# Kernel optimization log

Measured on AMD Instinct MI355X. Metric: run time of the kernel, lower is better.

Reference implementation:

```python
import jax, jax.numpy as jnp
import numpy as np

NEG_BIG = -9e15
ALPHA = 0.2  # leaky relu slope


def gat_layer(h, mask, W, a, concat):
    # h: [N, Fin], W: [Fin, Fout], a: [2*Fout], mask: [N, N] bool
    Wh = h @ W                                   # [N, Fout]
    d = W.shape[1]
    f1 = Wh @ a[:d]                              # [N]
    f2 = Wh @ a[d:]                              # [N]
    e = jax.nn.leaky_relu(f1[:, None] + f2[None, :], ALPHA)   # [N, N]
    e = jnp.where(mask, e, NEG_BIG)
    attn = jax.nn.softmax(e, axis=1)             # masked softmax over neighbors
    out = attn @ Wh                              # [N, Fout]
    return jax.nn.elu(out) if concat else out


def setup_inputs() -> dict:
    key = jax.random.key(0)
    ks = jax.random.split(key, 16)
    N, NFEAT, NHID, NCLASS, DEG_MAX, NHEADS = 4096, 512, 64, 16, 128, 8
    s = lambda fan_in: 1.0 / np.sqrt(fan_in)
    return {
        "x": jax.random.normal(ks[0], (N, NFEAT), jnp.float32),
        "adj": jax.random.randint(ks[1], (N, N), 0, 2, jnp.int32),
        "W_att": jax.random.normal(ks[2], (NHEADS, NFEAT, NHID), jnp.float32) * s(NFEAT),
        "a_att": jax.random.normal(ks[3], (NHEADS, 2 * NHID), jnp.float32) * s(2 * NHID),
        "W_out1": jax.random.normal(ks[4], (NHEADS * NHID, NCLASS), jnp.float32) * s(NHEADS * NHID),
        "a_out1": jax.random.normal(ks[5], (2 * NCLASS,), jnp.float32) * s(2 * NCLASS),
        "W_out2": jax.random.normal(ks[6], (NHEADS * NHID, NHID), jnp.float32) * s(NHEADS * NHID),
        "a_out2": jax.random.normal(ks[7], (2 * NHID,), jnp.float32) * s(2 * NHID),
        "W_down": jax.random.normal(ks[8], (NFEAT, NHID), jnp.float32) * s(NFEAT),
        "b_down": jnp.zeros((NHID,), jnp.float32),
        "w_deg": jax.random.normal(ks[9], (NHID, 1), jnp.float32) * s(NHID),
        "b_deg": jnp.zeros((1,), jnp.float32),
        "W_deg3": jax.random.normal(ks[10], (NHID, DEG_MAX), jnp.float32) * s(NHID),
        "b_deg3": jnp.zeros((DEG_MAX,), jnp.float32),
    }


def reference(x, adj, W_att, a_att, W_out1, a_out1, W_out2, a_out2,
              W_down, b_down, w_deg, b_deg, W_deg3, b_deg3):
    mask = adj > 0                                              # [N, N] bool
    original_x = x @ W_down + b_down                            # [N, nhid]
    # multi-head attention (dropout is identity in eval mode)
    heads = jax.vmap(lambda W, a: gat_layer(x, mask, W, a, True))(W_att, a_att)  # [H, N, nhid]
    h = jnp.transpose(heads, (1, 0, 2)).reshape(x.shape[0], -1)  # [N, H*nhid] == torch.cat(dim=1)
    classify_x = jax.nn.elu(gat_layer(h, mask, W_out1, a_out1, False))  # [N, nclass]
    z = gat_layer(h, mask, W_out2, a_out2, False) + original_x          # [N, nhid]
    result1 = jax.nn.log_softmax(classify_x, axis=1)            # [N, nclass]
    result2 = (z @ w_deg + b_deg)[:, 0]                         # [N]
    result3 = z @ W_deg3 + b_deg3                               # [N, degree_max]
    return (result1, result2, result3)
```

## Files before the change

kernel.cpp:

```cpp
#include <hip/hip_runtime.h>
#include <hip/hip_bf16.h>

#define L2E 1.44269504088896f

typedef __attribute__((ext_vector_type(8))) short short8v;
typedef __attribute__((ext_vector_type(8))) _Float16 half8v;
typedef __attribute__((ext_vector_type(4))) float float4v;

__device__ __forceinline__ void gld16(void* lds, const void* gp) {
    __builtin_amdgcn_global_load_lds(
        (const __attribute__((address_space(1))) unsigned int*)gp,
        (__attribute__((address_space(3))) unsigned int*)lds, 16, 0, 0);
}
__device__ __forceinline__ unsigned pkbf(float a, float b) {
    unsigned r;
    asm("v_cvt_pk_bf16_f32 %0, %1, %2" : "=v"(r) : "v"(a), "v"(b));
    return r;
}
__device__ __forceinline__ unsigned pkrtz(float a, float b) {
    unsigned r;
    asm("v_cvt_pkrtz_f16_f32 %0, %1, %2" : "=v"(r) : "v"(a), "v"(b));
    return r;
}
__device__ __forceinline__ unsigned pkmul(unsigned a, unsigned b) {
    unsigned r;
    asm("v_pk_mul_f16 %0, %1, %2" : "=v"(r) : "v"(a), "v"(b));
    return r;
}
__device__ __forceinline__ unsigned pkmax(unsigned a, unsigned b) {
    unsigned r;
    asm("v_pk_max_f16 %0, %1, %2" : "=v"(r) : "v"(a), "v"(b));
    return r;
}

__device__ __forceinline__ void tp_body(const float* __restrict__ src,
                                        unsigned short* __restrict__ dst,
                                        int M, int F, int j0, int f0, float (*t)[17]) {
    int tid = threadIdx.x;
    int rr = tid >> 2, c0 = (tid & 3) * 4;
    float4 v = *(const float4*)&src[(size_t)(j0 + rr) * F + f0 + c0];
    t[rr][c0 + 0] = v.x;
    t[rr][c0 + 1] = v.y;
    t[rr][c0 + 2] = v.z;
    t[rr][c0 + 3] = v.w;
    __syncthreads();
    int f = tid >> 4, jl = (tid & 15) * 4;
    ushort4 o;
    o.x = (unsigned short)(pkbf(t[jl + 0][f], 0.f) & 0xffff);
    o.y = (unsigned short)(pkbf(t[jl + 1][f], 0.f) & 0xffff);
    o.z = (unsigned short)(pkbf(t[jl + 2][f], 0.f) & 0xffff);
    o.w = (unsigned short)(pkbf(t[jl + 3][f], 0.f) & 0xffff);
    *(ushort4*)&dst[(size_t)(f0 + f) * M + j0 + jl] = o;
}

__global__ __launch_bounds__(256) void prep_k(const int* __restrict__ adj,
                                              unsigned long long* __restrict__ mask,
                                              const float* __restrict__ x,
                                              unsigned short* __restrict__ xb,
                                              const float* __restrict__ W_att,
                                              const float* __restrict__ W_down,
                                              const float* __restrict__ W_out2,
                                              const float* __restrict__ W_out1,
                                              const float* __restrict__ W_deg3,
                                              unsigned short* __restrict__ WT,
                                              unsigned short* __restrict__ Wd3T) {
    __shared__ float tbuf[64][17];
    int bx = blockIdx.x, tid = threadIdx.x;
    if (bx < 65536) {
        size_t idx = (size_t)bx * 256 + tid;
        unsigned long long b = __ballot(adj[idx] > 0);
        if ((tid & 63) == 0) mask[idx >> 6] = b;
    } else if (bx < 66560) {
        int i = (bx - 65536) * 256 + tid;
        float4 a = ((const float4*)x)[i * 2];
        float4 b = ((const float4*)x)[i * 2 + 1];
        uint4 o = {pkbf(a.x, a.y), pkbf(a.z, a.w), pkbf(b.x, b.y), pkbf(b.z, b.w)};
        ((uint4*)xb)[i] = o;
    } else if (bx < 66880) {
        int r = bx - 66560;
        int z = r >> 5, rr = r & 31;
        const float* src = (z < 8) ? W_att + (size_t)z * 512 * 64 : ((z == 8) ? W_down : W_out2);
        tp_body(src, WT + (size_t)z * 64 * 512, 512, 64, (rr & 7) * 64, (rr >> 3) * 16, tbuf);
    } else if (bx < 66888) {
        int r = bx - 66880;
        tp_body(W_out1, WT + (size_t)640 * 512, 512, 16, r * 64, 0, tbuf);
    } else {
        int r = bx - 66888;
        tp_body(W_deg3, Wd3T, 64, 128, 0, r * 16, tbuf);
    }
}

template <int BM, int BN, int OUTMODE>
__global__ __launch_bounds__(256) void gemmb_k(const __hip_bfloat16* __restrict__ A,
                                               const __hip_bfloat16* __restrict__ BtB,
                                               const float* __restrict__ bias,
                                               void* __restrict__ CB,
                                               int M, int N, int K) {
    constexpr int BK = 64;
    constexpr int MF = BM / 64;
    const int tid = threadIdx.x, lane = tid & 63, wv = tid >> 6;
    const int l16 = lane & 15, kq = lane >> 4;
    const int row0 = blockIdx.x * BM, col0 = blockIdx.y * BN;
    const size_t czs = (size_t)M * N;
    const __hip_bfloat16* Bt = BtB + (size_t)blockIdx.z * N * K;

    __shared__ __align__(16) __hip_bfloat16 As[2][BM][BK];

    auto stageA = [&](int k0, int b) {
#pragma unroll
        for (int c = 0; c < BM / 32; ++c) {
            int off = (tid + c * 256) * 16;
            int rr = off >> 7;
            int ch = (off >> 4) & 7;
            int chs = ch ^ (rr & 7);
            gld16((char*)&As[b][0][0] + off, A + (size_t)(row0 + rr) * K + k0 + chs * 8);
        }
    };

    float4v acc[MF][BN / 16];
#pragma unroll
    for (int mf = 0; mf < MF; ++mf)
#pragma unroll
        for (int nf = 0; nf < BN / 16; ++nf) acc[mf][nf] = (float4v){0.f, 0.f, 0.f, 0.f};

    const int rowb = wv * (BM / 4);
    const int nk = K / BK;
    stageA(0, 0);
    for (int t = 0; t < nk; ++t) {
        int k0 = t * BK, cur = t & 1;
        if (t + 1 < nk) stageA(k0 + BK, cur ^ 1);
        short8v bfr[BN / 16][2];
#pragma unroll
        for (int nf = 0; nf < BN / 16; ++nf)
#pragma unroll
            for (int ks = 0; ks < 2; ++ks)
                bfr[nf][ks] = *(const short8v*)(Bt + (size_t)(col0 + nf * 16 + l16) * K +
                                                k0 + ks * 32 + kq * 8);
        __syncthreads();
        const char* asb = (const char*)&As[cur][0][0];
#pragma unroll
        for (int ks = 0; ks < 2; ++ks) {
            short8v afr[MF];
#pragma unroll
            for (int mf = 0; mf < MF; ++mf) {
                int rr = rowb + mf * 16 + l16;
                afr[mf] = *(const short8v*)(asb + rr * 128 +
                                            ((ks * 64 + kq * 16) ^ ((rr & 7) << 4)));
            }
#pragma unroll
            for (int mf = 0; mf < MF; ++mf)
#pragma unroll
                for (int nf = 0; nf < BN / 16; ++nf)
                    acc[mf][nf] = __builtin_amdgcn_mfma_f32_16x16x32_bf16(
                        afr[mf], bfr[nf][ks], acc[mf][nf], 0, 0, 0);
        }
        __syncthreads();
    }

#pragma unroll
    for (int mf = 0; mf < MF; ++mf)
#pragma unroll
        for (int nf = 0; nf < BN / 16; ++nf) {
            int rb = row0 + rowb + mf * 16 + kq * 4;
            int col = col0 + nf * 16 + l16;
            if constexpr (OUTMODE == 0) {
                float bb = bias ? bias[col] : 0.f;
                float* C = (float*)CB + (size_t)blockIdx.z * czs;
#pragma unroll
                for (int e = 0; e < 4; ++e) C[(size_t)(rb + e) * N + col] = acc[mf][nf][e] + bb;
            } else {
                uint2 u = {pkrtz(acc[mf][nf][0], acc[mf][nf][1]),
                           pkrtz(acc[mf][nf][2], acc[mf][nf][3])};
                unsigned short* Ct = (unsigned short*)CB + (size_t)blockIdx.z * czs;
                *(uint2*)&Ct[(size_t)col * M + rb] = u;
            }
        }
}

__global__ __launch_bounds__(256) void fvh_k(const _Float16* __restrict__ WhT,
                                             const float* __restrict__ a,
                                             float* __restrict__ f1, float* __restrict__ f2) {
    int zz = blockIdx.y;
    const _Float16* W = WhT + (size_t)zz * 64 * 4096;
    const float* az = a + (size_t)zz * 128;
    int i = blockIdx.x * 256 + threadIdx.x;
    float s1 = 0.f, s2 = 0.f;
    for (int k = 0; k < 64; k++) {
        float ww = (float)W[(size_t)k * 4096 + i];
        s1 = fmaf(ww, az[k], s1);
        s2 = fmaf(ww, az[64 + k], s2);
    }
    f1[(size_t)zz * 4096 + i] = s1;
    f2[(size_t)zz * 4096 + i] = s2;
}

__global__ __launch_bounds__(256) void fvo_k(const _Float16* __restrict__ Wh12T,
                                             const float* __restrict__ a2,
                                             const float* __restrict__ a1,
                                             float* __restrict__ f1o, float* __restrict__ f2o) {
    int y = blockIdx.y;
    const _Float16* W = Wh12T + (y ? (size_t)64 * 4096 : 0);
    const float* a = y ? a1 : a2;
    int D = y ? 16 : 64;
    int i = blockIdx.x * 256 + threadIdx.x;
    float s1 = 0.f, s2 = 0.f;
    for (int k = 0; k < D; k++) {
        float ww = (float)W[(size_t)k * 4096 + i];
        s1 = fmaf(ww, a[k], s1);
        s2 = fmaf(ww, a[D + k], s2);
    }
    f1o[(size_t)y * 4096 + i] = s1;
    f2o[(size_t)y * 4096 + i] = s2;
}

__global__ __launch_bounds__(256) void rmaxpn_k(const float* __restrict__ f2B,
                                                float* __restrict__ M2out,
                                                uint2* __restrict__ pnB) {
    int z = blockIdx.x, tid = threadIdx.x;
    const float* f2 = f2B + (size_t)z * 4096;
    uint2* pn = pnB + (size_t)z * 2048;
    __shared__ float red[256];
    float m = -1e30f;
    for (int t = tid; t < 4096; t += 256) m = fmaxf(m, f2[t]);
    red[tid] = m;
    __syncthreads();
    for (int off = 128; off > 0; off >>= 1) {
        if (tid < off) red[tid] = fmaxf(red[tid], red[tid + off]);
        __syncthreads();
    }
    float M2 = red[0];
    if (tid == 0) M2out[z] = M2;
    for (int p = tid; p < 2048; p += 256) {
        float a0 = f2[2 * p] - M2, a1 = f2[2 * p + 1] - M2;
        uint2 q;
        q.x = pkrtz(exp2f(L2E * a0), exp2f(L2E * a1));
        q.y = pkrtz(exp2f(0.2f * L2E * a0), exp2f(0.2f * L2E * a1));
        pn[p] = q;
    }
}

template <int FOUT>
__device__ __forceinline__ void attn_body(const _Float16* __restrict__ wt,
                                          const float* __restrict__ f1p,
                                          const uint2* __restrict__ pnp, float M2,
                                          const unsigned* __restrict__ mask32,
                                          float* __restrict__ part, float* __restrict__ Zb,
                                          int i0, int jlo, int nt,
                                          char* psbase, unsigned long long* lut) {
    constexpr int NN = 4096, TJ = 128;
    constexpr int MF = (FOUT == 64) ? 2 : 1;
    constexpr int NF = (FOUT == 64) ? 2 : 1;
    const int tid = threadIdx.x, lane = tid & 63, wv = tid >> 6;
    const int jg = __builtin_amdgcn_readfirstlane(wv);
    const int l16 = lane & 15, kq = lane >> 4, r = lane;

    if (tid < 16) {
        unsigned lo = ((tid & 1) ? 0xFFFFu : 0u) | ((tid & 2) ? 0xFFFF0000u : 0u);
        unsigned hi = ((tid & 4) ? 0xFFFFu : 0u) | ((tid & 8) ? 0xFFFF0000u : 0u);
        lut[tid] = (unsigned long long)lo | ((unsigned long long)hi << 32);
    }

    float f1i = f1p[i0 + r];
    float t8 = 0.8f * (f1i + M2);
    unsigned Pp2, Nn2;
    {
        float Ppf = exp2f(L2E * fminf(0.f, t8));
        float Nnf = exp2f(-L2E * fmaxf(0.f, t8));
        Pp2 = pkrtz(Ppf, Ppf);
        Nn2 = pkrtz(Nnf, Nnf);
    }
    half8v ones;
#pragma unroll
    for (int k = 0; k < 8; ++k) ones[k] = (_Float16)1.0f;

    float4v acc[MF][NF], accz[MF];
#pragma unroll
    for (int mf = 0; mf < MF; ++mf) {
        accz[mf] = (float4v){0.f, 0.f, 0.f, 0.f};
#pragma unroll
        for (int nf = 0; nf < NF; ++nf) acc[mf][nf] = (float4v){0.f, 0.f, 0.f, 0.f};
    }

    const int rowb = (FOUT == 64) ? (wv & 1) * 32 : wv * 16;
    const int colb = (FOUT == 64) ? (wv >> 1) * 32 : 0;
    const int swz = (r & 7) << 4;
    const unsigned* mrowp = mask32 + (size_t)(i0 + r) * (NN >> 5) + (jlo >> 5) + jg;
    char* pd = psbase + r * 256;
    __syncthreads();

    for (int t = 0; t < nt; ++t) {
        int jt = jlo + t * TJ;
        unsigned mw = mrowp[t * 4];
        const uint2* pw = pnp + (jt >> 1) + jg * 16;
#pragma unroll
        for (int b = 0; b < 4; ++b) {
            unsigned long long m0 = lut[(mw >> (b * 8)) & 15];
            unsigned long long m1 = lut[(mw >> (b * 8 + 4)) & 15];
            uint2 q0 = pw[b * 4 + 0], q1 = pw[b * 4 + 1];
            uint2 q2 = pw[b * 4 + 2], q3 = pw[b * 4 + 3];
            uint4 w4;
            w4.x = pkmax(pkmul(Pp2, q0.x), pkmul(Nn2, q0.y)) & (unsigned)m0;
            w4.y = pkmax(pkmul(Pp2, q1.x), pkmul(Nn2, q1.y)) & (unsigned)(m0 >> 32);
            w4.z = pkmax(pkmul(Pp2, q2.x), pkmul(Nn2, q2.y)) & (unsigned)m1;
            w4.w = pkmax(pkmul(Pp2, q3.x), pkmul(Nn2, q3.y)) & (unsigned)(m1 >> 32);
            *(uint4*)(pd + ((jg * 64 + b * 16) ^ swz)) = w4;
        }
        __syncthreads();
        half8v bfr[4][NF];
#pragma unroll
        for (int kt = 0; kt < 4; ++kt)
#pragma unroll
            for (int nf = 0; nf < NF; ++nf)
                bfr[kt][nf] = *(const half8v*)(wt + (size_t)(colb + nf * 16 + l16) * NN +
                                               jt + kt * 32 + kq * 8);
#pragma unroll
        for (int kt = 0; kt < 4; ++kt) {
            half8v afr[MF];
#pragma unroll
            for (int mf = 0; mf < MF; ++mf) {
                int row = rowb + mf * 16 + l16;
                afr[mf] = *(const half8v*)(psbase + row * 256 +
                                           ((kt * 64 + kq * 16) ^ ((row & 7) << 4)));
            }
#pragma unroll
            for (int mf = 0; mf < MF; ++mf) {
                accz[mf] = __builtin_amdgcn_mfma_f32_16x16x32_f16(afr[mf], ones, accz[mf],
                                                                  0, 0, 0);
#pragma unroll
                for (int nf = 0; nf < NF; ++nf)
                    acc[mf][nf] = __builtin_amdgcn_mfma_f32_16x16x32_f16(
                        afr[mf], bfr[kt][nf], acc[mf][nf], 0, 0, 0);
            }
        }
        __syncthreads();
    }

#pragma unroll
    for (int mf = 0; mf < MF; ++mf)
#pragma unroll
        for (int nf = 0; nf < NF; ++nf) {
            int rbl = rowb + mf * 16 + kq * 4;
            int col = colb + nf * 16 + l16;
#pragma unroll
            for (int e = 0; e < 4; ++e)
                part[(size_t)(i0 + rbl + e) * FOUT + col] = acc[mf][nf][e];
        }
    if (colb == 0 && l16 == 0) {
#pragma unroll
        for (int mf = 0; mf < MF; ++mf)
#pragma unroll
            for (int e = 0; e < 4; ++e)
                Zb[i0 + rowb + mf * 16 + kq * 4 + e] = accz[mf][e];
    }
}

__global__ __launch_bounds__(256) void attnh_k(const _Float16* __restrict__ WhT,
                                               const float* __restrict__ f1h,
                                               const uint2* __restrict__ pnh,
                                               const float* __restrict__ M2,
                                               const unsigned* __restrict__ mask32,
                                               float* __restrict__ parth,
                                               float* __restrict__ Zh) {
    __shared__ __align__(16) char Ps[64 * 128 * 2];
    __shared__ unsigned long long lut[16];
    int head = blockIdx.y, chunk = blockIdx.z, slot = chunk * 8 + head;
    attn_body<64>(WhT + (size_t)head * 64 * 4096, f1h + (size_t)head * 4096,
                  pnh + (size_t)head * 2048, M2[head], mask32,
                  parth + (size_t)slot * 4096 * 64, Zh + (size_t)slot * 4096,
                  blockIdx.x * 64, chunk * 1024, 8, Ps, lut);
}

__global__ __launch_bounds__(256) void attno_k(const _Float16* __restrict__ Wh12T,
                                               const float* __restrict__ f1o,
                                               const uint2* __restrict__ pno,
                                               const float* __restrict__ M2,
                                               const unsigned* __restrict__ mask32,
                                               float* __restrict__ part2,
                                               float* __restrict__ Z2,
                                               float* __restrict__ part1,
                                               float* __restrict__ Z1) {
    __shared__ __align__(16) char Ps[64 * 128 * 2];
    __shared__ unsigned long long lut[16];
    int chunk = blockIdx.z;
    if (blockIdx.y == 0)
        attn_body<64>(Wh12T, f1o, pno, M2[8], mask32, part2 + (size_t)chunk * 4096 * 64,
                      Z2 + (size_t)chunk * 4096, blockIdx.x * 64, chunk * 256, 2, Ps, lut);
    else
        attn_body<16>(Wh12T + (size_t)64 * 4096, f1o + 4096, pno + 2048, M2[9], mask32,
                      part1 + (size_t)chunk * 4096 * 16, Z1 + (size_t)chunk * 4096,
                      blockIdx.x * 64, chunk * 256, 2, Ps, lut);
}

__global__ __launch_bounds__(256) void combH_k(const float* __restrict__ part,
                                               const float* __restrict__ Zp,
                                               unsigned short* __restrict__ hcb, int N) {
    int id = blockIdx.x * 256 + threadIdx.x;
    int i = id >> 9, hf = id & 511;
    int h = hf >> 6, f = hf & 63;
    float s = 0.f, Z = 0.f;
#pragma unroll
    for (int c = 0; c < 4; c++) {
        int slot = c * 8 + h;
        s += part[((size_t)slot * N + i) * 64 + f];
        Z += Zp[(size_t)slot * N + i];
    }
    float o = s / Z;
    o = (o > 0.f) ? o : (__expf(o) - 1.f);
    hcb[id] = (unsigned short)(pkbf(o, 0.f) & 0xffff);
}

__global__ __launch_bounds__(256) void comb2_k(const float* __restrict__ part,
                                               const float* __restrict__ Zp,
                                               const _Float16* __restrict__ origT,
                                               const float* __restrict__ bdown,
                                               float* __restrict__ zout,
                                               unsigned short* __restrict__ zb, int N) {
    int id = blockIdx.x * 256 + threadIdx.x;
    int i = id >> 6, f = id & 63;
    float Zs = 0.f, s = 0.f;
#pragma unroll
    for (int c = 0; c < 16; c++) Zs += Zp[(size_t)c * N + i];
#pragma unroll
    for (int c = 0; c < 16; c++) s += part[((size_t)c * N + i) * 64 + f];
    float v = s / Zs + (float)origT[(size_t)f * N + i] + bdown[f];
    zout[id] = v;
    zb[id] = (unsigned short)(pkbf(v, 0.f) & 0xffff);
}

__global__ __launch_bounds__(256) void c1fin_k(const float* __restrict__ part1,
                                               const float* __restrict__ Z1,
                                               const float* __restrict__ zbuf,
                                               const float* __restrict__ wd,
                                               const float* __restrict__ bd,
                                               float* __restrict__ out, int N) {
    int i = blockIdx.x * 256 + threadIdx.x;
    float Z = 0.f;
#pragma unroll
    for (int c = 0; c < 16; c++) Z += Z1[(size_t)c * N + i];
    float v[16];
    float m = -1e30f;
#pragma unroll
    for (int f = 0; f < 16; f++) {
        float s = 0.f;
#pragma unroll
        for (int c = 0; c < 16; c++) s += part1[((size_t)c * N + i) * 16 + f];
        float o = s / Z;
        o = (o > 0.f) ? o : (expf(o) - 1.f);
        v[f] = o;
        m = fmaxf(m, o);
    }
    float se = 0.f;
#pragma unroll
    for (int f = 0; f < 16; f++) se += expf(v[f] - m);
    float l = m + logf(se);
#pragma unroll
    for (int f = 0; f < 16; f++) out[(size_t)i * 16 + f] = v[f] - l;
    float s2 = bd[0];
#pragma unroll
    for (int k = 0; k < 64; k++) s2 = fmaf(zbuf[(size_t)i * 64 + k], wd[k], s2);
    out[(size_t)N * 16 + i] = s2;
}

extern "C" void kernel_launch(void* const* d_in, const int* in_sizes, int n_in,
                              void* d_out, int out_size, void* d_ws, size_t ws_size,
                              hipStream_t stream) {
    const float* x = (const float*)d_in[0];
    const int* adj = (const int*)d_in[1];
    const float* W_att = (const float*)d_in[2];
    const float* a_att = (const float*)d_in[3];
    const float* W_out1 = (const float*)d_in[4];
    const float* a_out1 = (const float*)d_in[5];
    const float* W_out2 = (const float*)d_in[6];
    const float* a_out2 = (const float*)d_in[7];
    const float* W_down = (const float*)d_in[8];
    const float* b_down = (const float*)d_in[9];
    const float* w_deg = (const float*)d_in[10];
    const float* b_deg = (const float*)d_in[11];
    const float* W_deg3 = (const float*)d_in[12];
    const float* b_deg3 = (const float*)d_in[13];
    float* out = (float*)d_out;

    constexpr int N = 4096, NF = 512, NH = 64, NC = 16, H = 8, DM = 128;

    char* wp = (char*)d_ws;
    auto alloc = [&](size_t b) {
        char* p = wp;
        wp += (b + 255) & ~(size_t)255;
        return p;
    };
    unsigned long long* mask = (unsigned long long*)alloc((size_t)N * N / 8);
    unsigned short* xb = (unsigned short*)alloc((size_t)N * NF * 2);
    unsigned short* WT = (unsigned short*)alloc((size_t)656 * NF * 2);
    unsigned short* Wd3T = (unsigned short*)alloc((size_t)DM * NH * 2);
    unsigned short* WhT = (unsigned short*)alloc((size_t)9 * NH * N * 2);
    float* f1h = (float*)alloc((size_t)H * N * 4);
    float* f2h = (float*)alloc((size_t)H * N * 4);
    uint2* pnh = (uint2*)alloc((size_t)H * 2048 * 8);
    float* M2 = (float*)alloc(256);
    float* parth = (float*)alloc((size_t)32 * N * NH * 4);
    float* Zh = (float*)alloc((size_t)32 * N * 4);
    unsigned short* hcb = (unsigned short*)alloc((size_t)N * NF * 2);
    unsigned short* Wh12T = (unsigned short*)alloc((size_t)80 * N * 2);
    float* f1o = (float*)alloc((size_t)2 * N * 4);
    float* f2o = (float*)alloc((size_t)2 * N * 4);
    uint2* pno = (uint2*)alloc((size_t)2 * 2048 * 8);
    float* zbuf = (float*)alloc((size_t)N * NH * 4);
    unsigned short* zb = (unsigned short*)alloc((size_t)N * NH * 2);

    float* part2 = parth;
    float* part1 = parth + (size_t)16 * N * NH;
    float* Z2 = Zh;
    float* Z1 = Zh + (size_t)16 * N;

    const unsigned* mask32 = (const unsigned*)mask;

    prep_k<<<66896, 256, 0, stream>>>(adj, mask, x, xb, W_att, W_down, W_out2, W_out1,
                                      W_deg3, WT, Wd3T);
    gemmb_k<128, 32, 1><<<dim3(N / 128, 2, 9), 256, 0, stream>>>(
        (const __hip_bfloat16*)xb, (const __hip_bfloat16*)WT, nullptr, WhT, N, NH, NF);
    fvh_k<<<dim3(16, H), 256, 0, stream>>>((const _Float16*)WhT, a_att, f1h, f2h);
    rmaxpn_k<<<H, 256, 0, stream>>>(f2h, M2, pnh);
    attnh_k<<<dim3(N / 64, H, 4), 256, 0, stream>>>((const _Float16*)WhT, f1h, pnh, M2,
                                                    mask32, parth, Zh);
    combH_k<<<(size_t)N * 512 / 256, 256, 0, stream>>>(parth, Zh, hcb, N);
    gemmb_k<64, 16, 1><<<dim3(N / 64, 5, 1), 256, 0, stream>>>(
        (const __hip_bfloat16*)hcb, (const __hip_bfloat16*)(WT + (size_t)9 * NH * NF),
        nullptr, Wh12T, N, 80, NF);
    fvo_k<<<dim3(16, 2), 256, 0, stream>>>((const _Float16*)Wh12T, a_out2, a_out1, f1o, f2o);
    rmaxpn_k<<<2, 256, 0, stream>>>(f2o, M2 + 8, pno);
    attno_k<<<dim3(N / 64, 2, 16), 256, 0, stream>>>((const _Float16*)Wh12T, f1o, pno, M2,
                                                     mask32, part2, Z2, part1, Z1);
    comb2_k<<<(size_t)N * 64 / 256, 256, 0, stream>>>(
        part2, Z2, (const _Float16*)(WhT + (size_t)8 * NH * N), b_down, zbuf, zb, N);
    c1fin_k<<<N / 256, 256, 0, stream>>>(part1, Z1, zbuf, w_deg, b_deg, out, N);
    gemmb_k<64, 64, 0><<<dim3(N / 64, DM / 64, 1), 256, 0, stream>>>(
        (const __hip_bfloat16*)zb, (const __hip_bfloat16*)Wd3T, b_deg3,
        out + (size_t)N * NC + N, N, DM, NH);
}
```

Baseline: 316.8 us.

## Build attention weights directly in MFMA A-fragment registers, drop LDS staging

The attention kernel no longer writes masked exp weights to LDS and reads them back. Each lane now computes the exact 8 fp16 weights it needs for its MFMA A operand straight from the mask and the precomputed exp tables. Each wave owns 16 rows and all output columns, which removes both per-tile barriers. The j-range split is halved (fewer chunks, twice the tiles each), shrinking the partial buffers and the combine passes. In exchange, B fragments (Wh^T) are loaded by every wave instead of being shared per column slice, which raises global/L2 traffic. Fewer blocks also means less parallelism.

```diff
diff --git a/kernel.cpp b/kernel.cpp
--- a/kernel.cpp
+++ b/kernel.cpp
@@ -246,21 +246,22 @@
                                           const unsigned* __restrict__ mask32,
                                           float* __restrict__ part, float* __restrict__ Zb,
                                           int i0, int jlo, int nt,
-                                          char* psbase, unsigned long long* lut) {
+                                          unsigned long long* lut) {
     constexpr int NN = 4096, TJ = 128;
-    constexpr int MF = (FOUT == 64) ? 2 : 1;
-    constexpr int NF = (FOUT == 64) ? 2 : 1;
+    constexpr int NF = FOUT / 16;
     const int tid = threadIdx.x, lane = tid & 63, wv = tid >> 6;
-    const int jg = __builtin_amdgcn_readfirstlane(wv);
-    const int l16 = lane & 15, kq = lane >> 4, r = lane;
+    const int l16 = lane & 15, kq = lane >> 4;
 
     if (tid < 16) {
         unsigned lo = ((tid & 1) ? 0xFFFFu : 0u) | ((tid & 2) ? 0xFFFF0000u : 0u);
         unsigned hi = ((tid & 4) ? 0xFFFFu : 0u) | ((tid & 8) ? 0xFFFF0000u : 0u);
         lut[tid] = (unsigned long long)lo | ((unsigned long long)hi << 32);
     }
-
-    float f1i = f1p[i0 + r];
+    __syncthreads();
+
+    const int row = wv * 16 + l16;
+    const int i = i0 + row;
+    float f1i = f1p[i];
     float t8 = 0.8f * (f1i + M2);
     unsigned Pp2, Nn2;
     {
@@ -273,84 +274,55 @@
 #pragma unroll
     for (int k = 0; k < 8; ++k) ones[k] = (_Float16)1.0f;
 
-    float4v acc[MF][NF], accz[MF];
-#pragma unroll
-    for (int mf = 0; mf < MF; ++mf) {
-        accz[mf] = (float4v){0.f, 0.f, 0.f, 0.f};
-#pragma unroll
-        for (int nf = 0; nf < NF; ++nf) acc[mf][nf] = (float4v){0.f, 0.f, 0.f, 0.f};
-    }
-
-    const int rowb = (FOUT == 64) ? (wv & 1) * 32 : wv * 16;
-    const int colb = (FOUT == 64) ? (wv >> 1) * 32 : 0;
-    const int swz = (r & 7) << 4;
-    const unsigned* mrowp = mask32 + (size_t)(i0 + r) * (NN >> 5) + (jlo >> 5) + jg;
-    char* pd = psbase + r * 256;
-    __syncthreads();
+    float4v acc[NF], accz;
+    accz = (float4v){0.f, 0.f, 0.f, 0.f};
+#pragma unroll
+    for (int nf = 0; nf < NF; ++nf) acc[nf] = (float4v){0.f, 0.f, 0.f, 0.f};
+
+    const uint4* mrow = (const uint4*)(mask32 + (size_t)i * (NN >> 5) + (jlo >> 5));
 
     for (int t = 0; t < nt; ++t) {
         int jt = jlo + t * TJ;
-        unsigned mw = mrowp[t * 4];
-        const uint2* pw = pnp + (jt >> 1) + jg * 16;
-#pragma unroll
-        for (int b = 0; b < 4; ++b) {
-            unsigned long long m0 = lut[(mw >> (b * 8)) & 15];
-            unsigned long long m1 = lut[(mw >> (b * 8 + 4)) & 15];
-            uint2 q0 = pw[b * 4 + 0], q1 = pw[b * 4 + 1];
-            uint2 q2 = pw[b * 4 + 2], q3 = pw[b * 4 + 3];
+        uint4 mword = mrow[t];
+        unsigned mws[4] = {mword.x, mword.y, mword.z, mword.w};
+#pragma unroll
+        for (int kt = 0; kt < 4; ++kt) {
+            unsigned m8 = (mws[kt] >> (kq * 8)) & 0xff;
+            const uint2* pw = pnp + ((jt + kt * 32 + kq * 8) >> 1);
+            uint4 qa = *(const uint4*)pw;
+            uint4 qb = *(const uint4*)(pw + 2);
+            unsigned long long m0 = lut[m8 & 15];
+            unsigned long long m1 = lut[m8 >> 4];
             uint4 w4;
-            w4.x = pkmax(pkmul(Pp2, q0.x), pkmul(Nn2, q0.y)) & (unsigned)m0;
-            w4.y = pkmax(pkmul(Pp2, q1.x), pkmul(Nn2, q1.y)) & (unsigned)(m0 >> 32);
-            w4.z = pkmax(pkmul(Pp2, q2.x), pkmul(Nn2, q2.y)) & (unsigned)m1;
-            w4.w = pkmax(pkmul(Pp2, q3.x), pkmul(Nn2, q3.y)) & (unsigned)(m1 >> 32);
-            *(uint4*)(pd + ((jg * 64 + b * 16) ^ swz)) = w4;
+            w4.x = pkmax(pkmul(Pp2, qa.x), pkmul(Nn2, qa.y)) & (unsigned)m0;
+            w4.y = pkmax(pkmul(Pp2, qa.z), pkmul(Nn2, qa.w)) & (unsigned)(m0 >> 32);
+            w4.z = pkmax(pkmul(Pp2, qb.x), pkmul(Nn2, qb.y)) & (unsigned)m1;
+            w4.w = pkmax(pkmul(Pp2, qb.z), pkmul(Nn2, qb.w)) & (unsigned)(m1 >> 32);
+            half8v afr = __builtin_bit_cast(half8v, w4);
+            half8v bfr[NF];
+#pragma unroll
+            for (int nf = 0; nf < NF; ++nf)
+                bfr[nf] = *(const half8v*)(wt + (size_t)(nf * 16 + l16) * NN +
+                                           jt + kt * 32 + kq * 8);
+            accz = __builtin_amdgcn_mfma_f32_16x16x32_f16(afr, ones, accz, 0, 0, 0);
+#pragma unroll
+            for (int nf = 0; nf < NF; ++nf)
+                acc[nf] = __builtin_amdgcn_mfma_f32_16x16x32_f16(afr, bfr[nf], acc[nf],
+                                                                 0, 0, 0);
         }
-        __syncthreads();
-        half8v bfr[4][NF];
-#pragma unroll
-        for (int kt = 0; kt < 4; ++kt)
-#pragma unroll
-            for (int nf = 0; nf < NF; ++nf)
-                bfr[kt][nf] = *(const half8v*)(wt + (size_t)(colb + nf * 16 + l16) * NN +
-                                               jt + kt * 32 + kq * 8);
-#pragma unroll
-        for (int kt = 0; kt < 4; ++kt) {
-            half8v afr[MF];
-#pragma unroll
-            for (int mf = 0; mf < MF; ++mf) {
-                int row = rowb + mf * 16 + l16;
-                afr[mf] = *(const half8v*)(psbase + row * 256 +
-                                           ((kt * 64 + kq * 16) ^ ((row & 7) << 4)));
-            }
-#pragma unroll
-            for (int mf = 0; mf < MF; ++mf) {
-                accz[mf] = __builtin_amdgcn_mfma_f32_16x16x32_f16(afr[mf], ones, accz[mf],
-                                                                  0, 0, 0);
-#pragma unroll
-                for (int nf = 0; nf < NF; ++nf)
-                    acc[mf][nf] = __builtin_amdgcn_mfma_f32_16x16x32_f16(
-                        afr[mf], bfr[kt][nf], acc[mf][nf], 0, 0, 0);
-            }
-        }
-        __syncthreads();
-    }
-
-#pragma unroll
-    for (int mf = 0; mf < MF; ++mf)
-#pragma unroll
-        for (int nf = 0; nf < NF; ++nf) {
-            int rbl = rowb + mf * 16 + kq * 4;
-            int col = colb + nf * 16 + l16;
-#pragma unroll
-            for (int e = 0; e < 4; ++e)
-                part[(size_t)(i0 + rbl + e) * FOUT + col] = acc[mf][nf][e];
-        }
-    if (colb == 0 && l16 == 0) {
-#pragma unroll
-        for (int mf = 0; mf < MF; ++mf)
-#pragma unroll
-            for (int e = 0; e < 4; ++e)
-                Zb[i0 + rowb + mf * 16 + kq * 4 + e] = accz[mf][e];
+    }
+
+#pragma unroll
+    for (int nf = 0; nf < NF; ++nf) {
+        int rb = i0 + wv * 16 + kq * 4;
+#pragma unroll
+        for (int e = 0; e < 4; ++e)
+            part[(size_t)(rb + e) * FOUT + nf * 16 + l16] = acc[nf][e];
+    }
+    if (l16 == 0) {
+        int rb = i0 + wv * 16 + kq * 4;
+#pragma unroll
+        for (int e = 0; e < 4; ++e) Zb[rb + e] = accz[e];
     }
 }
 
@@ -361,13 +333,12 @@
                                                const unsigned* __restrict__ mask32,
                                                float* __restrict__ parth,
                                                float* __restrict__ Zh) {
-    __shared__ __align__(16) char Ps[64 * 128 * 2];
     __shared__ unsigned long long lut[16];
     int head = blockIdx.y, chunk = blockIdx.z, slot = chunk * 8 + head;
     attn_body<64>(WhT + (size_t)head * 64 * 4096, f1h + (size_t)head * 4096,
                   pnh + (size_t)head * 2048, M2[head], mask32,
                   parth + (size_t)slot * 4096 * 64, Zh + (size_t)slot * 4096,
-                  blockIdx.x * 64, chunk * 1024, 8, Ps, lut);
+                  blockIdx.x * 64, chunk * 2048, 16, lut);
 }
 
 __global__ __launch_bounds__(256) void attno_k(const _Float16* __restrict__ Wh12T,
@@ -379,16 +350,15 @@
                                                float* __restrict__ Z2,
                                                float* __restrict__ part1,
                                                float* __restrict__ Z1) {
-    __shared__ __align__(16) char Ps[64 * 128 * 2];
     __shared__ unsigned long long lut[16];
     int chunk = blockIdx.z;
     if (blockIdx.y == 0)
         attn_body<64>(Wh12T, f1o, pno, M2[8], mask32, part2 + (size_t)chunk * 4096 * 64,
-                      Z2 + (size_t)chunk * 4096, blockIdx.x * 64, chunk * 256, 2, Ps, lut);
+                      Z2 + (size_t)chunk * 4096, blockIdx.x * 64, chunk * 512, 4, lut);
     else
         attn_body<16>(Wh12T + (size_t)64 * 4096, f1o + 4096, pno + 2048, M2[9], mask32,
                       part1 + (size_t)chunk * 4096 * 16, Z1 + (size_t)chunk * 4096,
-                      blockIdx.x * 64, chunk * 256, 2, Ps, lut);
+                      blockIdx.x * 64, chunk * 512, 4, lut);
 }
 
 __global__ __launch_bounds__(256) void combH_k(const float* __restrict__ part,
@@ -399,7 +369,7 @@
     int h = hf >> 6, f = hf & 63;
     float s = 0.f, Z = 0.f;
 #pragma unroll
-    for (int c = 0; c < 4; c++) {
+    for (int c = 0; c < 2; c++) {
         int slot = c * 8 + h;
         s += part[((size_t)slot * N + i) * 64 + f];
         Z += Zp[(size_t)slot * N + i];
@@ -419,9 +389,9 @@
     int i = id >> 6, f = id & 63;
     float Zs = 0.f, s = 0.f;
 #pragma unroll
-    for (int c = 0; c < 16; c++) Zs += Zp[(size_t)c * N + i];
-#pragma unroll
-    for (int c = 0; c < 16; c++) s += part[((size_t)c * N + i) * 64 + f];
+    for (int c = 0; c < 8; c++) Zs += Zp[(size_t)c * N + i];
+#pragma unroll
+    for (int c = 0; c < 8; c++) s += part[((size_t)c * N + i) * 64 + f];
     float v = s / Zs + (float)origT[(size_t)f * N + i] + bdown[f];
     zout[id] = v;
     zb[id] = (unsigned short)(pkbf(v, 0.f) & 0xffff);
@@ -436,14 +406,14 @@
     int i = blockIdx.x * 256 + threadIdx.x;
     float Z = 0.f;
 #pragma unroll
-    for (int c = 0; c < 16; c++) Z += Z1[(size_t)c * N + i];
+    for (int c = 0; c < 8; c++) Z += Z1[(size_t)c * N + i];
     float v[16];
     float m = -1e30f;
 #pragma unroll
     for (int f = 0; f < 16; f++) {
         float s = 0.f;
 #pragma unroll
-        for (int c = 0; c < 16; c++) s += part1[((size_t)c * N + i) * 16 + f];
+        for (int c = 0; c < 8; c++) s += part1[((size_t)c * N + i) * 16 + f];
         float o = s / Z;
         o = (o > 0.f) ? o : (expf(o) - 1.f);
         v[f] = o;
@@ -497,8 +467,8 @@
     float* f2h = (float*)alloc((size_t)H * N * 4);
     uint2* pnh = (uint2*)alloc((size_t)H * 2048 * 8);
     float* M2 = (float*)alloc(256);
-    float* parth = (float*)alloc((size_t)32 * N * NH * 4);
-    float* Zh = (float*)alloc((size_t)32 * N * 4);
+    float* parth = (float*)alloc((size_t)16 * N * NH * 4);
+    float* Zh = (float*)alloc((size_t)16 * N * 4);
     unsigned short* hcb = (unsigned short*)alloc((size_t)N * NF * 2);
     unsigned short* Wh12T = (unsigned short*)alloc((size_t)80 * N * 2);
     float* f1o = (float*)alloc((size_t)2 * N * 4);
@@ -508,9 +478,9 @@
     unsigned short* zb = (unsigned short*)alloc((size_t)N * NH * 2);
 
     float* part2 = parth;
-    float* part1 = parth + (size_t)16 * N * NH;
+    float* part1 = parth + (size_t)8 * N * NH;
     float* Z2 = Zh;
-    float* Z1 = Zh + (size_t)16 * N;
+    float* Z1 = Zh + (size_t)8 * N;
 
     const unsigned* mask32 = (const unsigned*)mask;
 
@@ -520,7 +490,7 @@
         (const __hip_bfloat16*)xb, (const __hip_bfloat16*)WT, nullptr, WhT, N, NH, NF);
     fvh_k<<<dim3(16, H), 256, 0, stream>>>((const _Float16*)WhT, a_att, f1h, f2h);
     rmaxpn_k<<<H, 256, 0, stream>>>(f2h, M2, pnh);
-    attnh_k<<<dim3(N / 64, H, 4), 256, 0, stream>>>((const _Float16*)WhT, f1h, pnh, M2,
+    attnh_k<<<dim3(N / 64, H, 2), 256, 0, stream>>>((const _Float16*)WhT, f1h, pnh, M2,
                                                     mask32, parth, Zh);
     combH_k<<<(size_t)N * 512 / 256, 256, 0, stream>>>(parth, Zh, hcb, N);
     gemmb_k<64, 16, 1><<<dim3(N / 64, 5, 1), 256, 0, stream>>>(
@@ -528,8 +498,8 @@
         nullptr, Wh12T, N, 80, NF);
     fvo_k<<<dim3(16, 2), 256, 0, stream>>>((const _Float16*)Wh12T, a_out2, a_out1, f1o, f2o);
     rmaxpn_k<<<2, 256, 0, stream>>>(f2o, M2 + 8, pno);
-    attno_k<<<dim3(N / 64, 2, 16), 256, 0, stream>>>((const _Float16*)Wh12T, f1o, pno, M2,
-                                                     mask32, part2, Z2, part1, Z1);
+    attno_k<<<dim3(N / 64, 2, 8), 256, 0, stream>>>((const _Float16*)Wh12T, f1o, pno, M2,
+                                                    mask32, part2, Z2, part1, Z1);
     comb2_k<<<(size_t)N * 64 / 256, 256, 0, stream>>>(
         part2, Z2, (const _Float16*)(WhT + (size_t)8 * NH * N), b_down, zbuf, zb, N);
     c1fin_k<<<N / 256, 256, 0, stream>>>(part1, Z1, zbuf, w_deg, b_deg, out, N);
```

New measurement: 394.7 us. 24.6% more time.

## Stage attention V tiles in LDS, pipeline P compute, compute Z with packed adds

Applied to the files above, without the earlier changes.

The attention body now stages the Wh^T tile into LDS with async global_load_lds and an XOR swizzle, instead of loading B fragments straight from global memory. The next tile's load and probability computation are issued right after the MFMA loop, so they overlap across iterations. The row-sum Z is built with packed f16 adds rather than an extra MFMA against a ones vector, and the P buffer is padded instead of swizzled. The j-range split is halved, with fewer chunks and longer loops, so the partial buffers and combine kernels shrink; this trades parallelism and adds f16 accumulation error in Z.

```diff
diff --git a/kernel.cpp b/kernel.cpp
--- a/kernel.cpp
+++ b/kernel.cpp
@@ -30,6 +30,11 @@
 __device__ __forceinline__ unsigned pkmax(unsigned a, unsigned b) {
     unsigned r;
     asm("v_pk_max_f16 %0, %1, %2" : "=v"(r) : "v"(a), "v"(b));
+    return r;
+}
+__device__ __forceinline__ unsigned pkadd(unsigned a, unsigned b) {
+    unsigned r;
+    asm("v_pk_add_f16 %0, %1, %2" : "=v"(r) : "v"(a), "v"(b));
     return r;
 }
 
@@ -246,10 +251,13 @@
                                           const unsigned* __restrict__ mask32,
                                           float* __restrict__ part, float* __restrict__ Zb,
                                           int i0, int jlo, int nt,
-                                          char* psbase, unsigned long long* lut) {
-    constexpr int NN = 4096, TJ = 128;
+                                          char* __restrict__ bsbase,
+                                          char* __restrict__ psbase,
+                                          unsigned long long* lut, float (*Zs)[4]) {
+    constexpr int NN = 4096, TJ = 128, PROW = 272;
     constexpr int MF = (FOUT == 64) ? 2 : 1;
     constexpr int NF = (FOUT == 64) ? 2 : 1;
+    constexpr int PW = (FOUT * TJ * 2) / 4096;
     const int tid = threadIdx.x, lane = tid & 63, wv = tid >> 6;
     const int jg = __builtin_amdgcn_readfirstlane(wv);
     const int l16 = lane & 15, kq = lane >> 4, r = lane;
@@ -269,29 +277,32 @@
         Pp2 = pkrtz(Ppf, Ppf);
         Nn2 = pkrtz(Nnf, Nnf);
     }
-    half8v ones;
-#pragma unroll
-    for (int k = 0; k < 8; ++k) ones[k] = (_Float16)1.0f;
-
-    float4v acc[MF][NF], accz[MF];
-#pragma unroll
-    for (int mf = 0; mf < MF; ++mf) {
-        accz[mf] = (float4v){0.f, 0.f, 0.f, 0.f};
+    float Z = 0.f;
+
+    float4v acc[MF][NF];
+#pragma unroll
+    for (int mf = 0; mf < MF; ++mf)
 #pragma unroll
         for (int nf = 0; nf < NF; ++nf) acc[mf][nf] = (float4v){0.f, 0.f, 0.f, 0.f};
-    }
 
     const int rowb = (FOUT == 64) ? (wv & 1) * 32 : wv * 16;
     const int colb = (FOUT == 64) ? (wv >> 1) * 32 : 0;
-    const int swz = (r & 7) << 4;
     const unsigned* mrowp = mask32 + (size_t)(i0 + r) * (NN >> 5) + (jlo >> 5) + jg;
-    char* pd = psbase + r * 256;
-    __syncthreads();
-
-    for (int t = 0; t < nt; ++t) {
-        int jt = jlo + t * TJ;
-        unsigned mw = mrowp[t * 4];
+
+    auto stage = [&](int jt) {
+#pragma unroll
+        for (int c = 0; c < PW; ++c) {
+            int q = wv * PW + c;
+            int rr = q * 4 + kq;
+            int ch = l16;
+            int chs = (ch & 8) | ((ch & 7) ^ (rr & 7));
+            gld16(bsbase + q * 1024, wt + (size_t)rr * NN + jt + chs * 8);
+        }
+    };
+
+    auto pcompute = [&](int jt, unsigned mw) {
         const uint2* pw = pnp + (jt >> 1) + jg * 16;
+        char* pd = psbase + r * PROW + jg * 64;
 #pragma unroll
         for (int b = 0; b < 4; ++b) {
             unsigned long long m0 = lut[(mw >> (b * 8)) & 15];
@@ -303,37 +314,57 @@
             w4.y = pkmax(pkmul(Pp2, q1.x), pkmul(Nn2, q1.y)) & (unsigned)(m0 >> 32);
             w4.z = pkmax(pkmul(Pp2, q2.x), pkmul(Nn2, q2.y)) & (unsigned)m1;
             w4.w = pkmax(pkmul(Pp2, q3.x), pkmul(Nn2, q3.y)) & (unsigned)(m1 >> 32);
-            *(uint4*)(pd + ((jg * 64 + b * 16) ^ swz)) = w4;
-        }
+            *(uint4*)(pd + b * 16) = w4;
+            unsigned s = pkadd(pkadd(w4.x, w4.y), pkadd(w4.z, w4.w));
+            float lo, hi;
+            asm("v_cvt_f32_f16 %0, %1" : "=v"(lo) : "v"(s));
+            asm("v_cvt_f32_f16 %0, %1" : "=v"(hi) : "v"(s >> 16));
+            Z += lo + hi;
+        }
+    };
+
+    stage(jlo);
+    __syncthreads();
+    pcompute(jlo, mrowp[0]);
+
+    for (int t = 0; t < nt; ++t) {
+        int jt = jlo + t * TJ;
         __syncthreads();
         half8v bfr[4][NF];
 #pragma unroll
         for (int kt = 0; kt < 4; ++kt)
 #pragma unroll
-            for (int nf = 0; nf < NF; ++nf)
-                bfr[kt][nf] = *(const half8v*)(wt + (size_t)(colb + nf * 16 + l16) * NN +
-                                               jt + kt * 32 + kq * 8);
+            for (int nf = 0; nf < NF; ++nf) {
+                int col = colb + nf * 16 + l16;
+                int cc = kt * 4 + kq;
+                int ccs = (cc & 8) | ((cc & 7) ^ (col & 7));
+                bfr[kt][nf] = *(const half8v*)(bsbase + col * 256 + ccs * 16);
+            }
 #pragma unroll
         for (int kt = 0; kt < 4; ++kt) {
             half8v afr[MF];
 #pragma unroll
             for (int mf = 0; mf < MF; ++mf) {
                 int row = rowb + mf * 16 + l16;
-                afr[mf] = *(const half8v*)(psbase + row * 256 +
-                                           ((kt * 64 + kq * 16) ^ ((row & 7) << 4)));
+                afr[mf] = *(const half8v*)(psbase + row * PROW + kt * 64 + kq * 16);
             }
 #pragma unroll
-            for (int mf = 0; mf < MF; ++mf) {
-                accz[mf] = __builtin_amdgcn_mfma_f32_16x16x32_f16(afr[mf], ones, accz[mf],
-                                                                  0, 0, 0);
+            for (int mf = 0; mf < MF; ++mf)
 #pragma unroll
                 for (int nf = 0; nf < NF; ++nf)
                     acc[mf][nf] = __builtin_amdgcn_mfma_f32_16x16x32_f16(
                         afr[mf], bfr[kt][nf], acc[mf][nf], 0, 0, 0);
-            }
         }
         __syncthreads();
-    }
+        if (t + 1 < nt) {
+            stage(jt + TJ);
+            pcompute(jt + TJ, mrowp[(t + 1) * 4]);
+        }
+    }
+
+    Zs[r][wv] = Z;
+    __syncthreads();
+    if (tid < 64) Zb[i0 + tid] = Zs[tid][0] + Zs[tid][1] + Zs[tid][2] + Zs[tid][3];
 
 #pragma unroll
     for (int mf = 0; mf < MF; ++mf)
@@ -345,50 +376,48 @@
             for (int e = 0; e < 4; ++e)
                 part[(size_t)(i0 + rbl + e) * FOUT + col] = acc[mf][nf][e];
         }
-    if (colb == 0 && l16 == 0) {
-#pragma unroll
-        for (int mf = 0; mf < MF; ++mf)
-#pragma unroll
-            for (int e = 0; e < 4; ++e)
-                Zb[i0 + rowb + mf * 16 + kq * 4 + e] = accz[mf][e];
-    }
-}
-
-__global__ __launch_bounds__(256) void attnh_k(const _Float16* __restrict__ WhT,
-                                               const float* __restrict__ f1h,
-                                               const uint2* __restrict__ pnh,
-                                               const float* __restrict__ M2,
-                                               const unsigned* __restrict__ mask32,
-                                               float* __restrict__ parth,
-                                               float* __restrict__ Zh) {
-    __shared__ __align__(16) char Ps[64 * 128 * 2];
+}
+
+__global__ __launch_bounds__(256, 4) void attnh_k(const _Float16* __restrict__ WhT,
+                                                  const float* __restrict__ f1h,
+                                                  const uint2* __restrict__ pnh,
+                                                  const float* __restrict__ M2,
+                                                  const unsigned* __restrict__ mask32,
+                                                  float* __restrict__ parth,
+                                                  float* __restrict__ Zh) {
+    __shared__ __align__(16) char Bs[64 * 256];
+    __shared__ __align__(16) char Ps[64 * 272];
     __shared__ unsigned long long lut[16];
+    __shared__ float Zs[64][4];
     int head = blockIdx.y, chunk = blockIdx.z, slot = chunk * 8 + head;
     attn_body<64>(WhT + (size_t)head * 64 * 4096, f1h + (size_t)head * 4096,
                   pnh + (size_t)head * 2048, M2[head], mask32,
                   parth + (size_t)slot * 4096 * 64, Zh + (size_t)slot * 4096,
-                  blockIdx.x * 64, chunk * 1024, 8, Ps, lut);
-}
-
-__global__ __launch_bounds__(256) void attno_k(const _Float16* __restrict__ Wh12T,
-                                               const float* __restrict__ f1o,
-                                               const uint2* __restrict__ pno,
-                                               const float* __restrict__ M2,
-                                               const unsigned* __restrict__ mask32,
-                                               float* __restrict__ part2,
-                                               float* __restrict__ Z2,
-                                               float* __restrict__ part1,
-                                               float* __restrict__ Z1) {
-    __shared__ __align__(16) char Ps[64 * 128 * 2];
+                  blockIdx.x * 64, chunk * 2048, 16, Bs, Ps, lut, Zs);
+}
+
+__global__ __launch_bounds__(256, 4) void attno_k(const _Float16* __restrict__ Wh12T,
+                                                  const float* __restrict__ f1o,
+                                                  const uint2* __restrict__ pno,
+                                                  const float* __restrict__ M2,
+                                                  const unsigned* __restrict__ mask32,
+                                                  float* __restrict__ part2,
+                                                  float* __restrict__ Z2,
+                                                  float* __restrict__ part1,
+                                                  float* __restrict__ Z1) {
+    __shared__ __align__(16) char Bs[64 * 256];
+    __shared__ __align__(16) char Ps[64 * 272];
     __shared__ unsigned long long lut[16];
+    __shared__ float Zs[64][4];
     int chunk = blockIdx.z;
     if (blockIdx.y == 0)
         attn_body<64>(Wh12T, f1o, pno, M2[8], mask32, part2 + (size_t)chunk * 4096 * 64,
-                      Z2 + (size_t)chunk * 4096, blockIdx.x * 64, chunk * 256, 2, Ps, lut);
+                      Z2 + (size_t)chunk * 4096, blockIdx.x * 64, chunk * 512, 4,
+                      Bs, Ps, lut, Zs);
     else
         attn_body<16>(Wh12T + (size_t)64 * 4096, f1o + 4096, pno + 2048, M2[9], mask32,
                       part1 + (size_t)chunk * 4096 * 16, Z1 + (size_t)chunk * 4096,
-                      blockIdx.x * 64, chunk * 256, 2, Ps, lut);
+                      blockIdx.x * 64, chunk * 512, 4, Bs, Ps, lut, Zs);
 }
 
 __global__ __launch_bounds__(256) void combH_k(const float* __restrict__ part,
@@ -399,7 +428,7 @@
     int h = hf >> 6, f = hf & 63;
     float s = 0.f, Z = 0.f;
 #pragma unroll
-    for (int c = 0; c < 4; c++) {
+    for (int c = 0; c < 2; c++) {
         int slot = c * 8 + h;
         s += part[((size_t)slot * N + i) * 64 + f];
         Z += Zp[(size_t)slot * N + i];
@@ -419,9 +448,9 @@
     int i = id >> 6, f = id & 63;
     float Zs = 0.f, s = 0.f;
 #pragma unroll
-    for (int c = 0; c < 16; c++) Zs += Zp[(size_t)c * N + i];
-#pragma unroll
-    for (int c = 0; c < 16; c++) s += part[((size_t)c * N + i) * 64 + f];
+    for (int c = 0; c < 8; c++) Zs += Zp[(size_t)c * N + i];
+#pragma unroll
+    for (int c = 0; c < 8; c++) s += part[((size_t)c * N + i) * 64 + f];
     float v = s / Zs + (float)origT[(size_t)f * N + i] + bdown[f];
     zout[id] = v;
     zb[id] = (unsigned short)(pkbf(v, 0.f) & 0xffff);
@@ -436,14 +465,14 @@
     int i = blockIdx.x * 256 + threadIdx.x;
     float Z = 0.f;
 #pragma unroll
-    for (int c = 0; c < 16; c++) Z += Z1[(size_t)c * N + i];
+    for (int c = 0; c < 8; c++) Z += Z1[(size_t)c * N + i];
     float v[16];
     float m = -1e30f;
 #pragma unroll
     for (int f = 0; f < 16; f++) {
         float s = 0.f;
 #pragma unroll
-        for (int c = 0; c < 16; c++) s += part1[((size_t)c * N + i) * 16 + f];
+        for (int c = 0; c < 8; c++) s += part1[((size_t)c * N + i) * 16 + f];
         float o = s / Z;
         o = (o > 0.f) ? o : (expf(o) - 1.f);
         v[f] = o;
@@ -497,8 +526,8 @@
     float* f2h = (float*)alloc((size_t)H * N * 4);
     uint2* pnh = (uint2*)alloc((size_t)H * 2048 * 8);
     float* M2 = (float*)alloc(256);
-    float* parth = (float*)alloc((size_t)32 * N * NH * 4);
-    float* Zh = (float*)alloc((size_t)32 * N * 4);
+    float* parth = (float*)alloc((size_t)16 * N * NH * 4);
+    float* Zh = (float*)alloc((size_t)16 * N * 4);
     unsigned short* hcb = (unsigned short*)alloc((size_t)N * NF * 2);
     unsigned short* Wh12T = (unsigned short*)alloc((size_t)80 * N * 2);
     float* f1o = (float*)alloc((size_t)2 * N * 4);
@@ -508,9 +537,9 @@
     unsigned short* zb = (unsigned short*)alloc((size_t)N * NH * 2);
 
     float* part2 = parth;
-    float* part1 = parth + (size_t)16 * N * NH;
+    float* part1 = parth + (size_t)8 * N * NH;
     float* Z2 = Zh;
-    float* Z1 = Zh + (size_t)16 * N;
+    float* Z1 = Zh + (size_t)8 * N;
 
     const unsigned* mask32 = (const unsigned*)mask;
 
@@ -520,7 +549,7 @@
         (const __hip_bfloat16*)xb, (const __hip_bfloat16*)WT, nullptr, WhT, N, NH, NF);
     fvh_k<<<dim3(16, H), 256, 0, stream>>>((const _Float16*)WhT, a_att, f1h, f2h);
     rmaxpn_k<<<H, 256, 0, stream>>>(f2h, M2, pnh);
-    attnh_k<<<dim3(N / 64, H, 4), 256, 0, stream>>>((const _Float16*)WhT, f1h, pnh, M2,
+    attnh_k<<<dim3(N / 64, H, 2), 256, 0, stream>>>((const _Float16*)WhT, f1h, pnh, M2,
                                                     mask32, parth, Zh);
     combH_k<<<(size_t)N * 512 / 256, 256, 0, stream>>>(parth, Zh, hcb, N);
     gemmb_k<64, 16, 1><<<dim3(N / 64, 5, 1), 256, 0, stream>>>(
@@ -528,8 +557,8 @@
         nullptr, Wh12T, N, 80, NF);
     fvo_k<<<dim3(16, 2), 256, 0, stream>>>((const _Float16*)Wh12T, a_out2, a_out1, f1o, f2o);
     rmaxpn_k<<<2, 256, 0, stream>>>(f2o, M2 + 8, pno);
-    attno_k<<<dim3(N / 64, 2, 16), 256, 0, stream>>>((const _Float16*)Wh12T, f1o, pno, M2,
-                                                     mask32, part2, Z2, part1, Z1);
+    attno_k<<<dim3(N / 64, 2, 8), 256, 0, stream>>>((const _Float16*)Wh12T, f1o, pno, M2,
+                                                    mask32, part2, Z2, part1, Z1);
     comb2_k<<<(size_t)N * 64 / 256, 256, 0, stream>>>(
         part2, Z2, (const _Float16*)(WhT + (size_t)8 * NH * N), b_down, zbuf, zb, N);
     c1fin_k<<<N / 256, 256, 0, stream>>>(part1, Z1, zbuf, w_deg, b_deg, out, N);
```

Result: faster. 274.6 us (-13.3%).
